# Optimization experiments

Measured on AMD Instinct MI355X. Metric: run time of the kernel, lower is better.

## Reference

```python
import jax, jax.numpy as jnp
import numpy as np

B, H, S, Dh = 4, 16, 2048, 64
NEG = -1.0e9


def setup_inputs() -> dict:
    key = jax.random.key(0)
    kq, kk, kv = jax.random.split(key, 3)
    q = jax.random.normal(kq, (B, H, S, Dh), dtype=jnp.float32)
    k = jax.random.normal(kk, (B, H, S, Dh), dtype=jnp.float32)
    v = jax.random.normal(kv, (B, H, S, Dh), dtype=jnp.float32)
    # causal mask: 1.0 where attention is disallowed (j > i), matching mask * -1e9
    mask = jnp.triu(jnp.ones((S, S), dtype=jnp.float32), k=1)[None, None, :, :]
    return {"q": q, "k": k, "v": v, "mask": mask}


def reference(q, k, v, mask):
    # scaled dot-product attention: softmax(QK^T / sqrt(Dh) + mask * -1e9) V
    dim_k = jnp.asarray(k.shape[-1], dtype=jnp.float32)
    logits = jnp.einsum("bhsd,bhtd->bhst", q, k) / jnp.sqrt(dim_k)
    logits = logits + mask * NEG
    weights = jax.nn.softmax(logits, axis=-1)
    return jnp.einsum("bhst,bhtd->bhsd", weights, v)
```

## Files before the change

### kernel.cpp

```cpp
#include <hip/hip_runtime.h>

#define S_LEN 2048
#define DH 64

typedef float f32x4 __attribute__((ext_vector_type(4)));
typedef __bf16 bf16x8 __attribute__((ext_vector_type(8)));
typedef unsigned u32x2v __attribute__((ext_vector_type(2)));

#define MFMA16(A, B, C) __builtin_amdgcn_mfma_f32_16x16x32_bf16(A, B, C, 0, 0, 0)

#ifdef __has_builtin
#if __has_builtin(__builtin_amdgcn_permlane16_swap) && __has_builtin(__builtin_amdgcn_permlane32_swap)
#define HAVE_PLSWAP 1
#endif
#if __has_builtin(__builtin_amdgcn_global_load_lds)
#define HAVE_GLDS 1
#endif
#if __has_builtin(__builtin_amdgcn_s_setprio)
#define SETPRIO(x) __builtin_amdgcn_s_setprio(x)
#endif
#endif
#ifndef HAVE_PLSWAP
#define HAVE_PLSWAP 0
#endif
#ifndef HAVE_GLDS
#define HAVE_GLDS 0
#endif
#ifndef SETPRIO
#define SETPRIO(x)
#endif

__device__ __forceinline__ unsigned short f2bf(float f) {
    unsigned u = __builtin_bit_cast(unsigned, f);
    u += 0x7fffu + ((u >> 16) & 1u);
    return (unsigned short)(u >> 16);
}

__device__ __forceinline__ uint4 pack8(const float* s) {
    unsigned short h[8];
#pragma unroll
    for (int i = 0; i < 8; ++i) h[i] = f2bf(s[i]);
    return *(const uint4*)h;
}

__device__ __forceinline__ unsigned pack_tr(float a, float b) {
    return __builtin_amdgcn_perm(__builtin_bit_cast(unsigned, b),
                                 __builtin_bit_cast(unsigned, a), 0x07060302u);
}

__device__ __forceinline__ bf16x8 ld128(const unsigned short* p) {
    return __builtin_bit_cast(bf16x8, *(const uint4*)p);
}

__device__ __forceinline__ bf16x8 ones8() {
    uint4 ou; ou.x = 0x3F803F80u; ou.y = ou.x; ou.z = ou.x; ou.w = ou.x;
    return __builtin_bit_cast(bf16x8, ou);
}

__device__ __forceinline__ void pl32pair(unsigned& x, unsigned& y) {
#if HAVE_PLSWAP
    u32x2v r = __builtin_amdgcn_permlane32_swap(x, y, false, false);
    x = r[0]; y = r[1];
#else
    unsigned sx = __shfl_xor(x, 32, 64);
    unsigned sy = __shfl_xor(y, 32, 64);
    const bool hi = (threadIdx.x & 32) != 0;
    unsigned nx = hi ? sy : x;
    unsigned ny = hi ? y : sx;
    x = nx; y = ny;
#endif
}

__device__ __forceinline__ void pl16pair(unsigned& x, unsigned& y) {
#if HAVE_PLSWAP
    u32x2v r = __builtin_amdgcn_permlane16_swap(x, y, false, false);
    x = r[0]; y = r[1];
#else
    unsigned sx = __shfl_xor(x, 16, 64);
    unsigned sy = __shfl_xor(y, 16, 64);
    const bool odd = (threadIdx.x & 16) != 0;
    unsigned nx = odd ? sy : x;
    unsigned ny = odd ? y : sx;
    x = nx; y = ny;
#endif
}

__device__ __forceinline__ bf16x8 frag_from(unsigned A0, unsigned B0,
                                            unsigned A1, unsigned B1) {
    pl32pair(A0, A1);
    pl16pair(A0, A1);
    pl32pair(B0, B1);
    pl16pair(B0, B1);
    uint4 u; u.x = A0; u.y = B0; u.z = A1; u.w = B1;
    return __builtin_bit_cast(bf16x8, u);
}

__device__ __forceinline__ void glds16(const uint4* g, unsigned short* l) {
#if HAVE_GLDS
    __builtin_amdgcn_global_load_lds(
        (const __attribute__((address_space(1))) uint4*)g,
        (__attribute__((address_space(3))) uint4*)l, 16, 0, 0);
#else
    *(uint4*)l = *g;
#endif
}

__global__ __launch_bounds__(256) void prep_kv(const float* __restrict__ k,
                                               const float* __restrict__ v,
                                               uint4* __restrict__ kimg,
                                               uint4* __restrict__ vimg) {
    __shared__ unsigned short tr[64 * 40];
    const int bid = blockIdx.x;
    const int t = threadIdx.x;
    if (bid < 4096) {
        const int r = t >> 3, b = t & 7;
        const int srcblk = b ^ (r & 7);
        const float* src = k + ((size_t)bid * 32 + r) * 64 + srcblk * 8;
        float buf[8];
        *(float4*)&buf[0] = *(const float4*)src;
        *(float4*)&buf[4] = *(const float4*)(src + 4);
        kimg[(size_t)bid * 256 + t] = pack8(buf);
    } else {
        const int vb = bid - 4096;
        const int r = t >> 3, cb = t & 7;
        const float* src = v + ((size_t)vb * 32 + r) * 64 + cb * 8;
        float buf[8];
        *(float4*)&buf[0] = *(const float4*)src;
        *(float4*)&buf[4] = *(const float4*)(src + 4);
#pragma unroll
        for (int i = 0; i < 8; ++i)
            tr[(cb * 8 + i) * 40 + r] = f2bf(buf[i]);
        __syncthreads();
        const int d = t >> 2, kb = t & 3;
        const int skb = kb ^ ((d >> 1) & 3);
        vimg[(size_t)vb * 256 + t] = *(const uint4*)&tr[d * 40 + skb * 8];
    }
}

template <bool MB>
__device__ __forceinline__ void body2(
    const unsigned short* __restrict__ kt_, const unsigned short* __restrict__ vt_,
    const bf16x8* qA, const bf16x8* qB,
    f32x4 (&accA)[4], f32x4 (&accB)[4], f32x4& aclA, f32x4& aclB,
    int igB, int kb, int quad, int c)
{
    const int sw = c & 7;
    const bf16x8 ones = ones8();
    const int f0 = (quad ^ sw) << 3;
    const int f1 = ((quad | 4) ^ sw) << 3;
    bf16x8 pfA[2], pfB[2];
#pragma unroll
    for (int h = 0; h < 2; ++h) {
        unsigned pA[2][2], pB[2][2];
#pragma unroll
        for (int m = 0; m < 2; ++m) {
            const int mt = 2 * h + m;
            const unsigned short* kr = kt_ + (mt * 16 + c) * 64;
            bf16x8 k0 = ld128(kr + f0), k1 = ld128(kr + f1);
            {
                f32x4 s = (f32x4){0.f, 0.f, 0.f, 0.f};
                s = MFMA16(k0, qA[0], s);
                s = MFMA16(k1, qA[1], s);
                float p[4];
#pragma unroll
                for (int r = 0; r < 4; ++r) p[r] = __builtin_amdgcn_exp2f(s[r]);
                pA[m][0] = pack_tr(p[0], p[1]);
                pA[m][1] = pack_tr(p[2], p[3]);
            }
            {
                f32x4 s = (f32x4){0.f, 0.f, 0.f, 0.f};
                s = MFMA16(k0, qB[0], s);
                s = MFMA16(k1, qB[1], s);
                float p[4];
#pragma unroll
                for (int r = 0; r < 4; ++r) {
                    float e = __builtin_amdgcn_exp2f(s[r]);
                    if (MB) {
                        const int jg = kb + mt * 16 + quad * 4 + r;
                        e = (jg > igB) ? 0.f : e;
                    }
                    p[r] = e;
                }
                pB[m][0] = pack_tr(p[0], p[1]);
                pB[m][1] = pack_tr(p[2], p[3]);
            }
        }
        pfA[h] = frag_from(pA[0][0], pA[0][1], pA[1][0], pA[1][1]);
        aclA = MFMA16(pfA[h], ones, aclA);
        pfB[h] = frag_from(pB[0][0], pB[0][1], pB[1][0], pB[1][1]);
        aclB = MFMA16(pfB[h], ones, aclB);
    }
    const int vsw = (c >> 1) & 3;
#pragma unroll
    for (int dc = 0; dc < 4; ++dc) {
        const int vo = (dc * 16 + c) * 32 + ((quad ^ vsw) << 3);
        bf16x8 v0 = ld128(vt_ + vo), v1 = ld128(vt_ + vo + 2048);
        accA[dc] = MFMA16(pfA[0], v0, accA[dc]);
        accA[dc] = MFMA16(pfA[1], v1, accA[dc]);
        accB[dc] = MFMA16(pfB[0], v0, accB[dc]);
        accB[dc] = MFMA16(pfB[1], v1, accB[dc]);
    }
}

template <bool MASK>
__device__ __forceinline__ void body1(
    const unsigned short* __restrict__ kt_, const unsigned short* __restrict__ vt_,
    const bf16x8* qA, f32x4 (&acc)[4], f32x4& acl,
    int ig, int kb, int quad, int c)
{
    const int sw = c & 7;
    const bf16x8 ones = ones8();
    const int f0 = (quad ^ sw) << 3;
    const int f1 = ((quad | 4) ^ sw) << 3;
    bf16x8 pf[2];
#pragma unroll
    for (int h = 0; h < 2; ++h) {
        unsigned pA[2][2];
#pragma unroll
        for (int m = 0; m < 2; ++m) {
            const int mt = 2 * h + m;
            const unsigned short* kr = kt_ + (mt * 16 + c) * 64;
            bf16x8 k0 = ld128(kr + f0), k1 = ld128(kr + f1);
            f32x4 s = (f32x4){0.f, 0.f, 0.f, 0.f};
            s = MFMA16(k0, qA[0], s);
            s = MFMA16(k1, qA[1], s);
            float p[4];
#pragma unroll
            for (int r = 0; r < 4; ++r) {
                float e = __builtin_amdgcn_exp2f(s[r]);
                if (MASK) {
                    const int jg = kb + mt * 16 + quad * 4 + r;
                    e = (jg > ig) ? 0.f : e;
                }
                p[r] = e;
            }
            pA[m][0] = pack_tr(p[0], p[1]);
            pA[m][1] = pack_tr(p[2], p[3]);
        }
        pf[h] = frag_from(pA[0][0], pA[0][1], pA[1][0], pA[1][1]);
        acl = MFMA16(pf[h], ones, acl);
    }
    const int vsw = (c >> 1) & 3;
#pragma unroll
    for (int dc = 0; dc < 4; ++dc) {
        const int vo = (dc * 16 + c) * 32 + ((quad ^ vsw) << 3);
        bf16x8 v0 = ld128(vt_ + vo), v1 = ld128(vt_ + vo + 2048);
        acc[dc] = MFMA16(pf[0], v0, acc[dc]);
        acc[dc] = MFMA16(pf[1], v1, acc[dc]);
    }
}

__device__ __forceinline__ void write_strip(float* __restrict__ ob,
                                            const f32x4* acc, const f32x4 acl,
                                            int rowbase, int quad, int c) {
    float linv[4];
#pragma unroll
    for (int r = 0; r < 4; ++r) linv[r] = 1.0f / acl[r];
#pragma unroll
    for (int dc = 0; dc < 4; ++dc)
#pragma unroll
        for (int r = 0; r < 4; ++r) {
            const size_t idx =
                (size_t)(rowbase + quad * 4 + r) * DH + dc * 16 + c;
            ob[idx] = acc[dc][r] * linv[r];
        }
}

__global__ __launch_bounds__(256, 4) void fa_kernel(
    const float* __restrict__ q,
    const uint4* __restrict__ kimg,
    const uint4* __restrict__ vimg,
    float* __restrict__ out)
{
    __shared__ unsigned short kt[2][64 * 64];
    __shared__ unsigned short vt[2][2 * 64 * 32];

    const int tid  = threadIdx.x;
    const int lane = tid & 63;
    const int wave = tid >> 6;
    const int quad = lane >> 4;
    const int c    = lane & 15;

    const int bid = blockIdx.x;
    const int bh  = bid & 63;
    const int ci  = bid >> 6;
    const int last = 31 - ci;
    const int hib = last * 64 + wave * 16;
    const int lob = ci * 64 + wave * 16;

    const size_t head_off = (size_t)bh * S_LEN * DH;

    const uint4* kin = kimg + (size_t)bh * 16384;
    const uint4* vin = vimg + (size_t)bh * 16384;

    auto stage = [&](int jt, int b) {
        const uint4* kg = kin + jt * 512 + tid;
        const uint4* vg = vin + jt * 512 + tid;
        glds16(kg,       &kt[b][0] + (size_t)tid * 8);
        glds16(kg + 256, &kt[b][0] + (size_t)(tid + 256) * 8);
        glds16(vg,       &vt[b][0] + (size_t)tid * 8);
        glds16(vg + 256, &vt[b][0] + (size_t)(tid + 256) * 8);
    };

    stage(0, 0);

    const float SCALE = 0.125f * 1.4426950408889634f;
    bf16x8 qf[4];
#pragma unroll
    for (int s = 0; s < 2; ++s) {
        const int base = s ? lob : hib;
        const float* qrow = q + head_off + (size_t)(base + c) * DH;
        float t0[8], t1[8];
#pragma unroll
        for (int i = 0; i < 8; ++i) t0[i] = qrow[quad * 8 + i] * SCALE;
#pragma unroll
        for (int i = 0; i < 8; ++i) t1[i] = qrow[32 + quad * 8 + i] * SCALE;
        qf[s * 2 + 0] = __builtin_bit_cast(bf16x8, pack8(t0));
        qf[s * 2 + 1] = __builtin_bit_cast(bf16x8, pack8(t1));
    }

    f32x4 accA[4], accB[4];
#pragma unroll
    for (int dc = 0; dc < 4; ++dc) {
        accA[dc] = (f32x4){0.f, 0.f, 0.f, 0.f};
        accB[dc] = (f32x4){0.f, 0.f, 0.f, 0.f};
    }
    f32x4 aclA = (f32x4){0.f, 0.f, 0.f, 0.f};
    f32x4 aclB = (f32x4){0.f, 0.f, 0.f, 0.f};

    const int igA = hib + c;
    const int igB = lob + c;

    int jt = 0;
    for (; jt <= ci; ++jt) {
        __syncthreads();
        if (jt < last) stage(jt + 1, (jt + 1) & 1);
        const unsigned short* K = kt[jt & 1];
        const unsigned short* V = vt[jt & 1];
        SETPRIO(1);
        if (jt < ci)
            body2<false>(K, V, qf, qf + 2, accA, accB, aclA, aclB,
                         igB, jt * 64, quad, c);
        else
            body2<true>(K, V, qf, qf + 2, accA, accB, aclA, aclB,
                        igB, jt * 64, quad, c);
        SETPRIO(0);
    }

    write_strip(out + head_off, accB, aclB, lob, quad, c);
#pragma unroll
    for (int dc = 0; dc < 4; ++dc) accB[dc] = (f32x4){0.f, 0.f, 0.f, 0.f};
    aclB = (f32x4){0.f, 0.f, 0.f, 0.f};

    for (; jt <= last; ++jt) {
        __syncthreads();
        if (jt < last) stage(jt + 1, (jt + 1) & 1);
        const unsigned short* K = kt[jt & 1];
        const unsigned short* V = vt[jt & 1];
        const int kb = jt * 64;
        SETPRIO(1);
        if ((jt ^ ci) & 1) {
            if (jt == last) body1<true >(K, V, qf, accB, aclB, igA, kb, quad, c);
            else            body1<false>(K, V, qf, accB, aclB, igA, kb, quad, c);
        } else {
            if (jt == last) body1<true >(K, V, qf, accA, aclA, igA, kb, quad, c);
            else            body1<false>(K, V, qf, accA, aclA, igA, kb, quad, c);
        }
        SETPRIO(0);
    }

#pragma unroll
    for (int dc = 0; dc < 4; ++dc) accA[dc] += accB[dc];
    aclA += aclB;
    write_strip(out + head_off, accA, aclA, hib, quad, c);
}

#define KT_STRIDE 88
#define VT_STRIDE 36
__global__ __launch_bounds__(256) void fa_kernel_fb(
    const float* __restrict__ q, const float* __restrict__ k,
    const float* __restrict__ v, float* __restrict__ out)
{
    __shared__ unsigned short kts[32 * KT_STRIDE];
    __shared__ unsigned short vts[64 * VT_STRIDE];
    __shared__ unsigned short pts[4][16 * 40];
    const int tid = threadIdx.x, lane = tid & 63, wave = tid >> 6;
    const int quad = lane >> 4, c = lane & 15;
    const int bid = blockIdx.x, bh = bid & 63, qblk = 31 - (bid >> 6);
    const int qtile = qblk * 4 + wave, qbase = qtile * 16;
    const int my_diag = qtile >> 1, jt_last = (qblk * 4 + 3) >> 1;
    const size_t head_off = (size_t)bh * S_LEN * DH;
    const float* qrow = q + head_off + (size_t)(qbase + c) * DH;
    float qtmp[8];
#pragma unroll
    for (int i = 0; i < 8; ++i) qtmp[i] = qrow[quad * 8 + i];
    bf16x8 qf0 = __builtin_bit_cast(bf16x8, pack8(qtmp));
#pragma unroll
    for (int i = 0; i < 8; ++i) qtmp[i] = qrow[32 + quad * 8 + i];
    bf16x8 qf1 = __builtin_bit_cast(bf16x8, pack8(qtmp));
    f32x4 acc[4];
#pragma unroll
    for (int dc = 0; dc < 4; ++dc) acc[dc] = (f32x4){0.f, 0.f, 0.f, 0.f};
    float m_run = -1e30f, l_run = 0.f;
    const int ig = qbase + c;
    const int srow = tid >> 3, sdb = tid & 7;
    const int vcol = (((srow >> 3) ^ (sdb & 3)) << 3) | (srow & 7);
    const float LOG2E = 1.4426950408889634f;
    for (int jt = 0; jt <= jt_last; ++jt) {
        __syncthreads();
        {
            const size_t g = head_off + (size_t)(jt * 32 + srow) * DH + sdb * 8;
            float kbuf[8];
            *(float4*)&kbuf[0] = *(const float4*)(k + g);
            *(float4*)&kbuf[4] = *(const float4*)(k + g + 4);
            *(uint4*)&kts[srow * KT_STRIDE + sdb * 8] = pack8(kbuf);
            float vbuf[8];
            *(float4*)&vbuf[0] = *(const float4*)(v + g);
            *(float4*)&vbuf[4] = *(const float4*)(v + g + 4);
#pragma unroll
            for (int i = 0; i < 8; ++i)
                vts[(sdb * 8 + i) * VT_STRIDE + vcol] = f2bf(vbuf[i]);
        }
        __syncthreads();
        if (jt > my_diag) continue;
        f32x4 st[2];
#pragma unroll
        for (int mt = 0; mt < 2; ++mt) {
            const unsigned short* krow = &kts[(mt * 16 + c) * KT_STRIDE + quad * 8];
            bf16x8 ka0 = __builtin_bit_cast(bf16x8, *(const uint4*)krow);
            bf16x8 ka1 = __builtin_bit_cast(bf16x8, *(const uint4*)(krow + 32));
            f32x4 a = (f32x4){0.f, 0.f, 0.f, 0.f};
            a = MFMA16(ka0, qf0, a);
            a = MFMA16(ka1, qf1, a);
            st[mt] = a;
        }
        float tv[8];
#pragma unroll
        for (int mt = 0; mt < 2; ++mt)
#pragma unroll
            for (int r = 0; r < 4; ++r) {
                const int jg = jt * 32 + mt * 16 + quad * 4 + r;
                const float s = st[mt][r] * 0.125f;
                tv[mt * 4 + r] = (jg > ig) ? -1e30f : s;
            }
        float tm = tv[0];
#pragma unroll
        for (int i = 1; i < 8; ++i) tm = fmaxf(tm, tv[i]);
        tm = fmaxf(tm, __shfl_xor(tm, 16, 64));
        tm = fmaxf(tm, __shfl_xor(tm, 32, 64));
        const float m_new = fmaxf(m_run, tm);
        const float mb = m_new * LOG2E;
        float p[8], ps = 0.f;
#pragma unroll
        for (int i = 0; i < 8; ++i) {
            p[i] = __builtin_amdgcn_exp2f(tv[i] * LOG2E - mb);
            ps += p[i];
        }
        ps += __shfl_xor(ps, 16, 64);
        ps += __shfl_xor(ps, 32, 64);
        const float alpha = __builtin_amdgcn_exp2f((m_run - m_new) * LOG2E);
        l_run = l_run * alpha + ps;
        m_run = m_new;
        unsigned short* pwf = pts[wave];
#pragma unroll
        for (int mt = 0; mt < 2; ++mt)
#pragma unroll
            for (int r = 0; r < 4; ++r)
                pwf[c * 40 + mt * 16 + quad * 4 + r] = f2bf(p[mt * 4 + r]);
        float ar[4];
#pragma unroll
        for (int r = 0; r < 4; ++r)
            ar[r] = __shfl(alpha, (quad << 4) + quad * 4 + r, 64);
#pragma unroll
        for (int dc = 0; dc < 4; ++dc)
#pragma unroll
            for (int r = 0; r < 4; ++r) acc[dc][r] *= ar[r];
        bf16x8 pf = __builtin_bit_cast(bf16x8, *(const uint4*)&pwf[c * 40 + quad * 8]);
#pragma unroll
        for (int dc = 0; dc < 4; ++dc) {
            const int vrow = dc * 16 + c;
            const int blk = quad ^ ((vrow >> 3) & 3);
            const unsigned short* vp = &vts[vrow * VT_STRIDE + blk * 8];
            uint2 a0 = *(const uint2*)vp;
            uint2 a1 = *(const uint2*)(vp + 4);
            uint4 u; u.x = a0.x; u.y = a0.y; u.z = a1.x; u.w = a1.y;
            bf16x8 vf = __builtin_bit_cast(bf16x8, u);
            acc[dc] = MFMA16(pf, vf, acc[dc]);
        }
    }
    float linv[4];
#pragma unroll
    for (int r = 0; r < 4; ++r) {
        const float lr = __shfl(l_run, (quad << 4) + quad * 4 + r, 64);
        linv[r] = 1.0f / lr;
    }
    float* ob = out + head_off;
#pragma unroll
    for (int dc = 0; dc < 4; ++dc)
#pragma unroll
        for (int r = 0; r < 4; ++r) {
            const size_t idx = (size_t)(qbase + quad * 4 + r) * DH + dc * 16 + c;
            ob[idx] = acc[dc][r] * linv[r];
        }
}

extern "C" void kernel_launch(void* const* d_in, const int* in_sizes, int n_in,
                              void* d_out, int out_size, void* d_ws, size_t ws_size,
                              hipStream_t stream) {
    const float* q = (const float*)d_in[0];
    const float* k = (const float*)d_in[1];
    const float* v = (const float*)d_in[2];
    float* o = (float*)d_out;
    const size_t need = (size_t)2 * 64 * 64 * 4096;
    if (ws_size >= need) {
        uint4* kimg = (uint4*)d_ws;
        uint4* vimg = kimg + (size_t)64 * 64 * 256;
        hipLaunchKernelGGL(prep_kv, dim3(8192), dim3(256), 0, stream, k, v, kimg, vimg);
        hipLaunchKernelGGL(fa_kernel, dim3(1024), dim3(256), 0, stream, q, kimg, vimg, o);
    } else {
        hipLaunchKernelGGL(fa_kernel_fb, dim3(2048), dim3(256), 0, stream, q, k, v, o);
    }
}
```

Baseline: 187.1 us.

## Fuse K/V bf16 image preparation into attention kernel with per-head counters

Removes the separate prep_kv launch. Each attention block now converts its own share of K and V rows into the swizzled bf16 images. It then bumps a per-head atomic counter and spin-waits until all 16 blocks of that head have finished before staging tiles. The intent is to remove the inter-kernel gap and overlap conversion with Q loading. In exchange it adds a memset of the counters, an inter-block spin barrier that needs all 1024 blocks to be co-resident, and global fences.

```diff
diff --git a/kernel.cpp b/kernel.cpp
--- a/kernel.cpp
+++ b/kernel.cpp
@@ -105,36 +105,33 @@
 #endif
 }
 
-__global__ __launch_bounds__(256) void prep_kv(const float* __restrict__ k,
-                                               const float* __restrict__ v,
-                                               uint4* __restrict__ kimg,
-                                               uint4* __restrict__ vimg) {
-    __shared__ unsigned short tr[64 * 40];
-    const int bid = blockIdx.x;
-    const int t = threadIdx.x;
-    if (bid < 4096) {
-        const int r = t >> 3, b = t & 7;
-        const int srcblk = b ^ (r & 7);
-        const float* src = k + ((size_t)bid * 32 + r) * 64 + srcblk * 8;
-        float buf[8];
-        *(float4*)&buf[0] = *(const float4*)src;
-        *(float4*)&buf[4] = *(const float4*)(src + 4);
-        kimg[(size_t)bid * 256 + t] = pack8(buf);
-    } else {
-        const int vb = bid - 4096;
-        const int r = t >> 3, cb = t & 7;
-        const float* src = v + ((size_t)vb * 32 + r) * 64 + cb * 8;
-        float buf[8];
-        *(float4*)&buf[0] = *(const float4*)src;
-        *(float4*)&buf[4] = *(const float4*)(src + 4);
-#pragma unroll
-        for (int i = 0; i < 8; ++i)
-            tr[(cb * 8 + i) * 40 + r] = f2bf(buf[i]);
-        __syncthreads();
-        const int d = t >> 2, kb = t & 3;
-        const int skb = kb ^ ((d >> 1) & 3);
-        vimg[(size_t)vb * 256 + t] = *(const uint4*)&tr[d * 40 + skb * 8];
-    }
+__device__ __forceinline__ void conv_k(const float* __restrict__ k,
+                                       uint4* __restrict__ kimg,
+                                       int hb, int t) {
+    const int r = t >> 3, b = t & 7;
+    const int srcblk = b ^ (r & 7);
+    const float* src = k + ((size_t)hb * 32 + r) * 64 + srcblk * 8;
+    float buf[8];
+    *(float4*)&buf[0] = *(const float4*)src;
+    *(float4*)&buf[4] = *(const float4*)(src + 4);
+    kimg[(size_t)hb * 256 + t] = pack8(buf);
+}
+
+__device__ __forceinline__ void conv_v(const float* __restrict__ v,
+                                       uint4* __restrict__ vimg,
+                                       int hb, int t, unsigned short* tr) {
+    const int r = t >> 3, cb = t & 7;
+    const float* src = v + ((size_t)hb * 32 + r) * 64 + cb * 8;
+    float buf[8];
+    *(float4*)&buf[0] = *(const float4*)src;
+    *(float4*)&buf[4] = *(const float4*)(src + 4);
+#pragma unroll
+    for (int i = 0; i < 8; ++i)
+        tr[(cb * 8 + i) * 40 + r] = f2bf(buf[i]);
+    __syncthreads();
+    const int d = t >> 2, kb2 = t & 3;
+    const int skb = kb2 ^ ((d >> 1) & 3);
+    vimg[(size_t)hb * 256 + t] = *(const uint4*)&tr[d * 40 + skb * 8];
 }
 
 template <bool MB>
@@ -268,8 +265,11 @@
 
 __global__ __launch_bounds__(256, 4) void fa_kernel(
     const float* __restrict__ q,
-    const uint4* __restrict__ kimg,
-    const uint4* __restrict__ vimg,
+    const float* __restrict__ kglob,
+    const float* __restrict__ vglob,
+    uint4* __restrict__ kimg,
+    uint4* __restrict__ vimg,
+    int* __restrict__ ctr,
     float* __restrict__ out)
 {
     __shared__ unsigned short kt[2][64 * 64];
@@ -289,6 +289,46 @@
     const int lob = ci * 64 + wave * 16;
 
     const size_t head_off = (size_t)bh * S_LEN * DH;
+
+    {
+        unsigned short* tr = &kt[0][0];
+        const int base = bh * 64 + ci * 4;
+#pragma unroll
+        for (int u = 0; u < 4; ++u) conv_k(kglob, kimg, base + u, tid);
+#pragma unroll
+        for (int u = 0; u < 4; ++u) {
+            conv_v(vglob, vimg, base + u, tid, tr);
+            __syncthreads();
+        }
+        __threadfence();
+        __syncthreads();
+        if (tid == 0)
+            __hip_atomic_fetch_add(&ctr[bh], 1, __ATOMIC_RELEASE,
+                                   __HIP_MEMORY_SCOPE_AGENT);
+    }
+
+    const float SCALE = 0.125f * 1.4426950408889634f;
+    bf16x8 qf[4];
+#pragma unroll
+    for (int s = 0; s < 2; ++s) {
+        const int base = s ? lob : hib;
+        const float* qrow = q + head_off + (size_t)(base + c) * DH;
+        float t0[8], t1[8];
+#pragma unroll
+        for (int i = 0; i < 8; ++i) t0[i] = qrow[quad * 8 + i] * SCALE;
+#pragma unroll
+        for (int i = 0; i < 8; ++i) t1[i] = qrow[32 + quad * 8 + i] * SCALE;
+        qf[s * 2 + 0] = __builtin_bit_cast(bf16x8, pack8(t0));
+        qf[s * 2 + 1] = __builtin_bit_cast(bf16x8, pack8(t1));
+    }
+
+    if (tid == 0) {
+        while (__hip_atomic_load(&ctr[bh], __ATOMIC_ACQUIRE,
+                                 __HIP_MEMORY_SCOPE_AGENT) < 16)
+            __builtin_amdgcn_s_sleep(2);
+    }
+    __syncthreads();
+    __threadfence();
 
     const uint4* kin = kimg + (size_t)bh * 16384;
     const uint4* vin = vimg + (size_t)bh * 16384;
@@ -303,21 +343,6 @@
     };
 
     stage(0, 0);
-
-    const float SCALE = 0.125f * 1.4426950408889634f;
-    bf16x8 qf[4];
-#pragma unroll
-    for (int s = 0; s < 2; ++s) {
-        const int base = s ? lob : hib;
-        const float* qrow = q + head_off + (size_t)(base + c) * DH;
-        float t0[8], t1[8];
-#pragma unroll
-        for (int i = 0; i < 8; ++i) t0[i] = qrow[quad * 8 + i] * SCALE;
-#pragma unroll
-        for (int i = 0; i < 8; ++i) t1[i] = qrow[32 + quad * 8 + i] * SCALE;
-        qf[s * 2 + 0] = __builtin_bit_cast(bf16x8, pack8(t0));
-        qf[s * 2 + 1] = __builtin_bit_cast(bf16x8, pack8(t1));
-    }
 
     f32x4 accA[4], accB[4];
 #pragma unroll
@@ -511,12 +536,15 @@
     const float* k = (const float*)d_in[1];
     const float* v = (const float*)d_in[2];
     float* o = (float*)d_out;
-    const size_t need = (size_t)2 * 64 * 64 * 4096;
+    const size_t img_bytes = (size_t)2 * 64 * 64 * 4096;
+    const size_t need = img_bytes + 256;
     if (ws_size >= need) {
         uint4* kimg = (uint4*)d_ws;
         uint4* vimg = kimg + (size_t)64 * 64 * 256;
-        hipLaunchKernelGGL(prep_kv, dim3(8192), dim3(256), 0, stream, k, v, kimg, vimg);
-        hipLaunchKernelGGL(fa_kernel, dim3(1024), dim3(256), 0, stream, q, kimg, vimg, o);
+        int* ctr = (int*)((char*)d_ws + img_bytes);
+        hipMemsetAsync(ctr, 0, 256, stream);
+        hipLaunchKernelGGL(fa_kernel, dim3(1024), dim3(256), 0, stream,
+                           q, k, v, kimg, vimg, ctr, o);
     } else {
         hipLaunchKernelGGL(fa_kernel_fb, dim3(2048), dim3(256), 0, stream, q, k, v, o);
     }
```

After: 489.6 us. +161.6%, slower.

## Fuse K/V bf16 conversion into attention kernel with register-staged prefetch

Applied to the files above, without the earlier changes.

Removes the separate prep_kv pass that converted K and V to swizzled bf16 images in workspace. The attention kernel now loads fp32 K/V tiles into registers one tile ahead, then converts, packs and writes them (V transposed) into swizzled shared memory. V's swizzle gains an extra XOR term to cut bank conflicts on the scattered transpose stores. This drops a kernel launch and a full workspace round trip, but each block re-reads and re-converts the fp32 data, which doubles global load bytes and raises register pressure. It also replaces async global-to-LDS loads with synchronous register staging.

```diff
diff --git a/kernel.cpp b/kernel.cpp
--- a/kernel.cpp
+++ b/kernel.cpp
@@ -13,18 +13,12 @@
 #if __has_builtin(__builtin_amdgcn_permlane16_swap) && __has_builtin(__builtin_amdgcn_permlane32_swap)
 #define HAVE_PLSWAP 1
 #endif
-#if __has_builtin(__builtin_amdgcn_global_load_lds)
-#define HAVE_GLDS 1
-#endif
 #if __has_builtin(__builtin_amdgcn_s_setprio)
 #define SETPRIO(x) __builtin_amdgcn_s_setprio(x)
 #endif
 #endif
 #ifndef HAVE_PLSWAP
 #define HAVE_PLSWAP 0
-#endif
-#ifndef HAVE_GLDS
-#define HAVE_GLDS 0
 #endif
 #ifndef SETPRIO
 #define SETPRIO(x)
@@ -95,47 +89,6 @@
     return __builtin_bit_cast(bf16x8, u);
 }
 
-__device__ __forceinline__ void glds16(const uint4* g, unsigned short* l) {
-#if HAVE_GLDS
-    __builtin_amdgcn_global_load_lds(
-        (const __attribute__((address_space(1))) uint4*)g,
-        (__attribute__((address_space(3))) uint4*)l, 16, 0, 0);
-#else
-    *(uint4*)l = *g;
-#endif
-}
-
-__global__ __launch_bounds__(256) void prep_kv(const float* __restrict__ k,
-                                               const float* __restrict__ v,
-                                               uint4* __restrict__ kimg,
-                                               uint4* __restrict__ vimg) {
-    __shared__ unsigned short tr[64 * 40];
-    const int bid = blockIdx.x;
-    const int t = threadIdx.x;
-    if (bid < 4096) {
-        const int r = t >> 3, b = t & 7;
-        const int srcblk = b ^ (r & 7);
-        const float* src = k + ((size_t)bid * 32 + r) * 64 + srcblk * 8;
-        float buf[8];
-        *(float4*)&buf[0] = *(const float4*)src;
-        *(float4*)&buf[4] = *(const float4*)(src + 4);
-        kimg[(size_t)bid * 256 + t] = pack8(buf);
-    } else {
-        const int vb = bid - 4096;
-        const int r = t >> 3, cb = t & 7;
-        const float* src = v + ((size_t)vb * 32 + r) * 64 + cb * 8;
-        float buf[8];
-        *(float4*)&buf[0] = *(const float4*)src;
-        *(float4*)&buf[4] = *(const float4*)(src + 4);
-#pragma unroll
-        for (int i = 0; i < 8; ++i)
-            tr[(cb * 8 + i) * 40 + r] = f2bf(buf[i]);
-        __syncthreads();
-        const int d = t >> 2, kb = t & 3;
-        const int skb = kb ^ ((d >> 1) & 3);
-        vimg[(size_t)vb * 256 + t] = *(const uint4*)&tr[d * 40 + skb * 8];
-    }
-}
 
 template <bool MB>
 __device__ __forceinline__ void body2(
@@ -190,10 +143,11 @@
         pfB[h] = frag_from(pB[0][0], pB[0][1], pB[1][0], pB[1][1]);
         aclB = MFMA16(pfB[h], ones, aclB);
     }
-    const int vsw = (c >> 1) & 3;
 #pragma unroll
     for (int dc = 0; dc < 4; ++dc) {
-        const int vo = (dc * 16 + c) * 32 + ((quad ^ vsw) << 3);
+        const int d = dc * 16 + c;
+        const int vsw = ((d >> 1) & 3) ^ ((d >> 3) & 3);
+        const int vo = d * 32 + ((quad ^ vsw) << 3);
         bf16x8 v0 = ld128(vt_ + vo), v1 = ld128(vt_ + vo + 2048);
         accA[dc] = MFMA16(pfA[0], v0, accA[dc]);
         accA[dc] = MFMA16(pfA[1], v1, accA[dc]);
@@ -240,10 +194,11 @@
         pf[h] = frag_from(pA[0][0], pA[0][1], pA[1][0], pA[1][1]);
         acl = MFMA16(pf[h], ones, acl);
     }
-    const int vsw = (c >> 1) & 3;
 #pragma unroll
     for (int dc = 0; dc < 4; ++dc) {
-        const int vo = (dc * 16 + c) * 32 + ((quad ^ vsw) << 3);
+        const int d = dc * 16 + c;
+        const int vsw = ((d >> 1) & 3) ^ ((d >> 3) & 3);
+        const int vo = d * 32 + ((quad ^ vsw) << 3);
         bf16x8 v0 = ld128(vt_ + vo), v1 = ld128(vt_ + vo + 2048);
         acc[dc] = MFMA16(pf[0], v0, acc[dc]);
         acc[dc] = MFMA16(pf[1], v1, acc[dc]);
@@ -268,8 +223,8 @@
 
 __global__ __launch_bounds__(256, 4) void fa_kernel(
     const float* __restrict__ q,
-    const uint4* __restrict__ kimg,
-    const uint4* __restrict__ vimg,
+    const float* __restrict__ kg,
+    const float* __restrict__ vg,
     float* __restrict__ out)
 {
     __shared__ unsigned short kt[2][64 * 64];
@@ -290,19 +245,43 @@
 
     const size_t head_off = (size_t)bh * S_LEN * DH;
 
-    const uint4* kin = kimg + (size_t)bh * 16384;
-    const uint4* vin = vimg + (size_t)bh * 16384;
-
-    auto stage = [&](int jt, int b) {
-        const uint4* kg = kin + jt * 512 + tid;
-        const uint4* vg = vin + jt * 512 + tid;
-        glds16(kg,       &kt[b][0] + (size_t)tid * 8);
-        glds16(kg + 256, &kt[b][0] + (size_t)(tid + 256) * 8);
-        glds16(vg,       &vt[b][0] + (size_t)tid * 8);
-        glds16(vg + 256, &vt[b][0] + (size_t)(tid + 256) * 8);
+    const int sr = tid >> 3;
+    const int sb = tid & 7;
+    const float* kbase = kg + head_off + sb * 8;
+    const float* vbase = vg + head_off + sb * 8;
+
+    float kr0[8], kr1[8], vr0[8], vr1[8];
+
+    auto LOAD = [&](int jt) {
+        const size_t o0 = (size_t)(jt * 64 + sr) * 64;
+        const size_t o1 = o0 + 32 * 64;
+        *(float4*)&kr0[0] = *(const float4*)(kbase + o0);
+        *(float4*)&kr0[4] = *(const float4*)(kbase + o0 + 4);
+        *(float4*)&kr1[0] = *(const float4*)(kbase + o1);
+        *(float4*)&kr1[4] = *(const float4*)(kbase + o1 + 4);
+        *(float4*)&vr0[0] = *(const float4*)(vbase + o0);
+        *(float4*)&vr0[4] = *(const float4*)(vbase + o0 + 4);
+        *(float4*)&vr1[0] = *(const float4*)(vbase + o1);
+        *(float4*)&vr1[4] = *(const float4*)(vbase + o1 + 4);
     };
 
-    stage(0, 0);
+    auto WRITE = [&](int b) {
+        const int kcol = (sb ^ (sr & 7)) << 3;
+        *(uint4*)&kt[b][sr * 64 + kcol]        = pack8(kr0);
+        *(uint4*)&kt[b][(sr + 32) * 64 + kcol] = pack8(kr1);
+        const int kb4 = sr >> 3;
+        const int k7  = sr & 7;
+#pragma unroll
+        for (int i = 0; i < 8; ++i) {
+            const int d = sb * 8 + i;
+            const int j = kb4 ^ ((d >> 1) & 3) ^ ((d >> 3) & 3);
+            unsigned short* p = &vt[b][d * 32 + j * 8 + k7];
+            p[0]    = f2bf(vr0[i]);
+            p[2048] = f2bf(vr1[i]);
+        }
+    };
+
+    LOAD(0);
 
     const float SCALE = 0.125f * 1.4426950408889634f;
     bf16x8 qf[4];
@@ -319,6 +298,9 @@
         qf[s * 2 + 1] = __builtin_bit_cast(bf16x8, pack8(t1));
     }
 
+    WRITE(0);
+    LOAD(1 <= last ? 1 : 0);
+
     f32x4 accA[4], accB[4];
 #pragma unroll
     for (int dc = 0; dc < 4; ++dc) {
@@ -334,7 +316,10 @@
     int jt = 0;
     for (; jt <= ci; ++jt) {
         __syncthreads();
-        if (jt < last) stage(jt + 1, (jt + 1) & 1);
+        if (jt < last) {
+            WRITE((jt + 1) & 1);
+            LOAD(jt + 2 <= last ? jt + 2 : last);
+        }
         const unsigned short* K = kt[jt & 1];
         const unsigned short* V = vt[jt & 1];
         SETPRIO(1);
@@ -354,7 +339,10 @@
 
     for (; jt <= last; ++jt) {
         __syncthreads();
-        if (jt < last) stage(jt + 1, (jt + 1) & 1);
+        if (jt < last) {
+            WRITE((jt + 1) & 1);
+            LOAD(jt + 2 <= last ? jt + 2 : last);
+        }
         const unsigned short* K = kt[jt & 1];
         const unsigned short* V = vt[jt & 1];
         const int kb = jt * 64;
@@ -375,135 +363,6 @@
     write_strip(out + head_off, accA, aclA, hib, quad, c);
 }
 
-#define KT_STRIDE 88
-#define VT_STRIDE 36
-__global__ __launch_bounds__(256) void fa_kernel_fb(
-    const float* __restrict__ q, const float* __restrict__ k,
-    const float* __restrict__ v, float* __restrict__ out)
-{
-    __shared__ unsigned short kts[32 * KT_STRIDE];
-    __shared__ unsigned short vts[64 * VT_STRIDE];
-    __shared__ unsigned short pts[4][16 * 40];
-    const int tid = threadIdx.x, lane = tid & 63, wave = tid >> 6;
-    const int quad = lane >> 4, c = lane & 15;
-    const int bid = blockIdx.x, bh = bid & 63, qblk = 31 - (bid >> 6);
-    const int qtile = qblk * 4 + wave, qbase = qtile * 16;
-    const int my_diag = qtile >> 1, jt_last = (qblk * 4 + 3) >> 1;
-    const size_t head_off = (size_t)bh * S_LEN * DH;
-    const float* qrow = q + head_off + (size_t)(qbase + c) * DH;
-    float qtmp[8];
-#pragma unroll
-    for (int i = 0; i < 8; ++i) qtmp[i] = qrow[quad * 8 + i];
-    bf16x8 qf0 = __builtin_bit_cast(bf16x8, pack8(qtmp));
-#pragma unroll
-    for (int i = 0; i < 8; ++i) qtmp[i] = qrow[32 + quad * 8 + i];
-    bf16x8 qf1 = __builtin_bit_cast(bf16x8, pack8(qtmp));
-    f32x4 acc[4];
-#pragma unroll
-    for (int dc = 0; dc < 4; ++dc) acc[dc] = (f32x4){0.f, 0.f, 0.f, 0.f};
-    float m_run = -1e30f, l_run = 0.f;
-    const int ig = qbase + c;
-    const int srow = tid >> 3, sdb = tid & 7;
-    const int vcol = (((srow >> 3) ^ (sdb & 3)) << 3) | (srow & 7);
-    const float LOG2E = 1.4426950408889634f;
-    for (int jt = 0; jt <= jt_last; ++jt) {
-        __syncthreads();
-        {
-            const size_t g = head_off + (size_t)(jt * 32 + srow) * DH + sdb * 8;
-            float kbuf[8];
-            *(float4*)&kbuf[0] = *(const float4*)(k + g);
-            *(float4*)&kbuf[4] = *(const float4*)(k + g + 4);
-            *(uint4*)&kts[srow * KT_STRIDE + sdb * 8] = pack8(kbuf);
-            float vbuf[8];
-            *(float4*)&vbuf[0] = *(const float4*)(v + g);
-            *(float4*)&vbuf[4] = *(const float4*)(v + g + 4);
-#pragma unroll
-            for (int i = 0; i < 8; ++i)
-                vts[(sdb * 8 + i) * VT_STRIDE + vcol] = f2bf(vbuf[i]);
-        }
-        __syncthreads();
-        if (jt > my_diag) continue;
-        f32x4 st[2];
-#pragma unroll
-        for (int mt = 0; mt < 2; ++mt) {
-            const unsigned short* krow = &kts[(mt * 16 + c) * KT_STRIDE + quad * 8];
-            bf16x8 ka0 = __builtin_bit_cast(bf16x8, *(const uint4*)krow);
-            bf16x8 ka1 = __builtin_bit_cast(bf16x8, *(const uint4*)(krow + 32));
-            f32x4 a = (f32x4){0.f, 0.f, 0.f, 0.f};
-            a = MFMA16(ka0, qf0, a);
-            a = MFMA16(ka1, qf1, a);
-            st[mt] = a;
-        }
-        float tv[8];
-#pragma unroll
-        for (int mt = 0; mt < 2; ++mt)
-#pragma unroll
-            for (int r = 0; r < 4; ++r) {
-                const int jg = jt * 32 + mt * 16 + quad * 4 + r;
-                const float s = st[mt][r] * 0.125f;
-                tv[mt * 4 + r] = (jg > ig) ? -1e30f : s;
-            }
-        float tm = tv[0];
-#pragma unroll
-        for (int i = 1; i < 8; ++i) tm = fmaxf(tm, tv[i]);
-        tm = fmaxf(tm, __shfl_xor(tm, 16, 64));
-        tm = fmaxf(tm, __shfl_xor(tm, 32, 64));
-        const float m_new = fmaxf(m_run, tm);
-        const float mb = m_new * LOG2E;
-        float p[8], ps = 0.f;
-#pragma unroll
-        for (int i = 0; i < 8; ++i) {
-            p[i] = __builtin_amdgcn_exp2f(tv[i] * LOG2E - mb);
-            ps += p[i];
-        }
-        ps += __shfl_xor(ps, 16, 64);
-        ps += __shfl_xor(ps, 32, 64);
-        const float alpha = __builtin_amdgcn_exp2f((m_run - m_new) * LOG2E);
-        l_run = l_run * alpha + ps;
-        m_run = m_new;
-        unsigned short* pwf = pts[wave];
-#pragma unroll
-        for (int mt = 0; mt < 2; ++mt)
-#pragma unroll
-            for (int r = 0; r < 4; ++r)
-                pwf[c * 40 + mt * 16 + quad * 4 + r] = f2bf(p[mt * 4 + r]);
-        float ar[4];
-#pragma unroll
-        for (int r = 0; r < 4; ++r)
-            ar[r] = __shfl(alpha, (quad << 4) + quad * 4 + r, 64);
-#pragma unroll
-        for (int dc = 0; dc < 4; ++dc)
-#pragma unroll
-            for (int r = 0; r < 4; ++r) acc[dc][r] *= ar[r];
-        bf16x8 pf = __builtin_bit_cast(bf16x8, *(const uint4*)&pwf[c * 40 + quad * 8]);
-#pragma unroll
-        for (int dc = 0; dc < 4; ++dc) {
-            const int vrow = dc * 16 + c;
-            const int blk = quad ^ ((vrow >> 3) & 3);
-            const unsigned short* vp = &vts[vrow * VT_STRIDE + blk * 8];
-            uint2 a0 = *(const uint2*)vp;
-            uint2 a1 = *(const uint2*)(vp + 4);
-            uint4 u; u.x = a0.x; u.y = a0.y; u.z = a1.x; u.w = a1.y;
-            bf16x8 vf = __builtin_bit_cast(bf16x8, u);
-            acc[dc] = MFMA16(pf, vf, acc[dc]);
-        }
-    }
-    float linv[4];
-#pragma unroll
-    for (int r = 0; r < 4; ++r) {
-        const float lr = __shfl(l_run, (quad << 4) + quad * 4 + r, 64);
-        linv[r] = 1.0f / lr;
-    }
-    float* ob = out + head_off;
-#pragma unroll
-    for (int dc = 0; dc < 4; ++dc)
-#pragma unroll
-        for (int r = 0; r < 4; ++r) {
-            const size_t idx = (size_t)(qbase + quad * 4 + r) * DH + dc * 16 + c;
-            ob[idx] = acc[dc][r] * linv[r];
-        }
-}
-
 extern "C" void kernel_launch(void* const* d_in, const int* in_sizes, int n_in,
                               void* d_out, int out_size, void* d_ws, size_t ws_size,
                               hipStream_t stream) {
@@ -511,13 +370,5 @@
     const float* k = (const float*)d_in[1];
     const float* v = (const float*)d_in[2];
     float* o = (float*)d_out;
-    const size_t need = (size_t)2 * 64 * 64 * 4096;
-    if (ws_size >= need) {
-        uint4* kimg = (uint4*)d_ws;
-        uint4* vimg = kimg + (size_t)64 * 64 * 256;
-        hipLaunchKernelGGL(prep_kv, dim3(8192), dim3(256), 0, stream, k, v, kimg, vimg);
-        hipLaunchKernelGGL(fa_kernel, dim3(1024), dim3(256), 0, stream, q, kimg, vimg, o);
-    } else {
-        hipLaunchKernelGGL(fa_kernel_fb, dim3(2048), dim3(256), 0, stream, q, k, v, o);
-    }
-}
+    hipLaunchKernelGGL(fa_kernel, dim3(1024), dim3(256), 0, stream, q, k, v, o);
+}
```

Result: slower. 300.0 us (+60.3%).
